# Kernel optimization log

Hardware: AMD Instinct MI355X
Metric: run time of the kernel (lower is better)

## Reference

```python
import jax, jax.numpy as jnp
import numpy as np

H, W, WS, HEADS = 112, 112, 7, 8
DIM, HID = 512, 2048


def _layernorm(x, g, b, eps=1e-5):
    mu = jnp.mean(x, axis=-1, keepdims=True)
    var = jnp.var(x, axis=-1, keepdims=True)
    return (x - mu) * jax.lax.rsqrt(var + eps) * g + b


def _cpe(x, w, b):
    # depthwise 3x3 conv positional encoding with residual; x: [B, L, C]
    B, L, C = x.shape
    img = x.reshape(B, H, W, C)
    feat = jax.lax.conv_general_dilated(
        img, w, window_strides=(1, 1), padding='SAME',
        dimension_numbers=('NHWC', 'HWIO', 'NHWC'), feature_group_count=C) + b
    return x + feat.reshape(B, L, C)


def _window_partition(x):
    # [B, H, W, C] -> [B*nW, ws*ws, C]
    B, _, _, C = x.shape
    x = x.reshape(B, H // WS, WS, W // WS, WS, C)
    x = jnp.transpose(x, (0, 1, 3, 2, 4, 5))
    return x.reshape(-1, WS * WS, C)


def _window_reverse(xw, B):
    # [B*nW, ws*ws, C] -> [B, H*W, C]
    C = xw.shape[-1]
    x = xw.reshape(B, H // WS, W // WS, WS, WS, C)
    x = jnp.transpose(x, (0, 1, 3, 2, 4, 5))
    return x.reshape(B, H * W, C)


def _attention(x, qkv_w, qkv_b, proj_w, proj_b):
    # x: [nW, N, C]; standard MHA within each window
    nW, N, C = x.shape
    d = C // HEADS
    qkv = x @ qkv_w + qkv_b                      # [nW, N, 3C]
    qkv = qkv.reshape(nW, N, 3, HEADS, d)
    q, k, v = qkv[:, :, 0], qkv[:, :, 1], qkv[:, :, 2]  # [nW, N, h, d]
    scale = d ** -0.5
    attn = jnp.einsum('wqhd,wkhd->whqk', q * scale, k)
    attn = jax.nn.softmax(attn, axis=-1)
    out = jnp.einsum('whqk,wkhd->wqhd', attn, v).reshape(nW, N, C)
    return out @ proj_w + proj_b


def setup_inputs() -> dict:
    key = jax.random.key(0)
    ks = jax.random.split(key, 16)
    s = 0.02
    return {
        'x': jax.random.normal(ks[0], (4, H * W, DIM), jnp.float32),
        'cpe0_w': jax.random.normal(ks[1], (3, 3, 1, DIM), jnp.float32) * s,
        'cpe0_b': jnp.zeros((DIM,), jnp.float32),
        'cpe1_w': jax.random.normal(ks[2], (3, 3, 1, DIM), jnp.float32) * s,
        'cpe1_b': jnp.zeros((DIM,), jnp.float32),
        'ln1_g': jnp.ones((DIM,), jnp.float32),
        'ln1_b': jnp.zeros((DIM,), jnp.float32),
        'ln2_g': jnp.ones((DIM,), jnp.float32),
        'ln2_b': jnp.zeros((DIM,), jnp.float32),
        'qkv_w': jax.random.normal(ks[3], (DIM, 3 * DIM), jnp.float32) * s,
        'qkv_b': jnp.zeros((3 * DIM,), jnp.float32),
        'attn_proj_w': jax.random.normal(ks[4], (DIM, DIM), jnp.float32) * s,
        'attn_proj_b': jnp.zeros((DIM,), jnp.float32),
        'fc1_w': jax.random.normal(ks[5], (DIM, HID), jnp.float32) * s,
        'fc1_b': jnp.zeros((HID,), jnp.float32),
        'fc2_w': jax.random.normal(ks[6], (HID, DIM), jnp.float32) * s,
        'fc2_b': jnp.zeros((DIM,), jnp.float32),
    }


def reference(x, cpe0_w, cpe0_b, cpe1_w, cpe1_b, ln1_g, ln1_b, ln2_g, ln2_b,
              qkv_w, qkv_b, attn_proj_w, attn_proj_b, fc1_w, fc1_b, fc2_w, fc2_b):
    B, L, C = x.shape
    shortcut = _cpe(x, cpe0_w, cpe0_b)                 # CPE #1 (with residual)
    h = _layernorm(shortcut, ln1_g, ln1_b)
    h = _window_partition(h.reshape(B, H, W, C))       # [B*nW, 49, C]
    h = _attention(h, qkv_w, qkv_b, attn_proj_w, attn_proj_b)
    h = _window_reverse(h, B)                          # [B, L, C]
    h = shortcut + h
    h = _cpe(h, cpe1_w, cpe1_b)                        # CPE #2 (with residual)
    m = _layernorm(h, ln2_g, ln2_b)
    m = jax.nn.gelu(m @ fc1_w + fc1_b) @ fc2_w + fc2_b
    return h + m
```

## Files before the change

kernel.cpp:

```cpp
#include <hip/hip_runtime.h>
#include <stdint.h>

#define HH 112
#define WW 112
#define CC 512
#define BB 4
#define LLEN (HH*WW)
#define NTOK (BB*LLEN)
#define NHEADS 8
#define HD 64
#define HIDDEN 2048

typedef __bf16 bf16x8 __attribute__((ext_vector_type(8)));
typedef float f32x4 __attribute__((ext_vector_type(4)));
typedef int i32x8 __attribute__((ext_vector_type(8)));
typedef long i64;

__device__ __forceinline__ unsigned short f2bf(float x) {
  uint32_t u = __float_as_uint(x);
  u += 0x7fffu + ((u >> 16) & 1u);
  return (unsigned short)(u >> 16);
}
__device__ __forceinline__ float bf2f(unsigned short h) {
  return __uint_as_float((uint32_t)h << 16);
}
__device__ __forceinline__ int cvt4_fp8(float a, float b, float c, float d) {
  int r = 0;
  r = __builtin_amdgcn_cvt_pk_fp8_f32(a, b, r, false);
  r = __builtin_amdgcn_cvt_pk_fp8_f32(c, d, r, true);
  return r;
}

__device__ __forceinline__ void gload16(const void* gptr, void* lptr) {
  __builtin_amdgcn_global_load_lds(
      (const __attribute__((address_space(1))) void*)gptr,
      (__attribute__((address_space(3))) void*)lptr,
      16, 0, 0);
}

#define WAITV3() asm volatile("s_waitcnt vmcnt(3)" ::: "memory")
#define WAITV4() asm volatile("s_waitcnt vmcnt(4)" ::: "memory")
#define WAITV0() asm volatile("s_waitcnt vmcnt(0)" ::: "memory")
#define BAR() __builtin_amdgcn_s_barrier()
#define WAITL() do { asm volatile("s_waitcnt lgkmcnt(0)" ::: "memory"); \
                     __builtin_amdgcn_sched_barrier(0); } while (0)

__global__ __launch_bounds__(256) void wtranspose8_kernel(
    const float* __restrict__ w, unsigned char* __restrict__ wt, int K, int N) {
  int idx = blockIdx.x * 256 + threadIdx.x;
  if (idx >= K * N) return;
  int n = idx / K, k = idx - n * K;
  float v = w[(size_t)k * N + n] * 32.f;
  int r = __builtin_amdgcn_cvt_pk_fp8_f32(v, v, 0, false);
  wt[idx] = (unsigned char)r;
}

template <int INBF, int OUTBF>
__global__ __launch_bounds__(256) void cpe_ln_kernel(
    const void* __restrict__ xin, const float* __restrict__ w,
    const float* __restrict__ bias, const float* __restrict__ lng,
    const float* __restrict__ lnb, void* __restrict__ outp,
    unsigned char* __restrict__ ln8) {
  const int wid = threadIdx.x >> 6;
  const int lane = threadIdx.x & 63;
  const int xx = blockIdx.x * 4 + wid;
  const int yy = blockIdx.y;
  const int bb = blockIdx.z;
  const int c = lane * 8;

  float acc[8];
  {
    float4 b0 = *(const float4*)(&bias[c]);
    float4 b1 = *(const float4*)(&bias[c + 4]);
    acc[0] = b0.x; acc[1] = b0.y; acc[2] = b0.z; acc[3] = b0.w;
    acc[4] = b1.x; acc[5] = b1.y; acc[6] = b1.z; acc[7] = b1.w;
  }
  float xv[8];

  #pragma unroll
  for (int ky = 0; ky < 3; ky++) {
    int y = yy + ky - 1;
    bool yok = (unsigned)y < (unsigned)HH;
    #pragma unroll
    for (int kx = 0; kx < 3; kx++) {
      int x2 = xx + kx - 1;
      bool ok = yok && ((unsigned)x2 < (unsigned)WW);
      float v[8];
      if (ok) {
        size_t eo = (((size_t)bb * HH + y) * WW + x2) * CC + c;
        if (INBF) {
          uint4 u = *(const uint4*)(&((const unsigned short*)xin)[eo]);
          v[0] = bf2f((unsigned short)(u.x & 0xffff)); v[1] = bf2f((unsigned short)(u.x >> 16));
          v[2] = bf2f((unsigned short)(u.y & 0xffff)); v[3] = bf2f((unsigned short)(u.y >> 16));
          v[4] = bf2f((unsigned short)(u.z & 0xffff)); v[5] = bf2f((unsigned short)(u.z >> 16));
          v[6] = bf2f((unsigned short)(u.w & 0xffff)); v[7] = bf2f((unsigned short)(u.w >> 16));
        } else {
          float4 a = *(const float4*)(&((const float*)xin)[eo]);
          float4 b = *(const float4*)(&((const float*)xin)[eo + 4]);
          v[0] = a.x; v[1] = a.y; v[2] = a.z; v[3] = a.w;
          v[4] = b.x; v[5] = b.y; v[6] = b.z; v[7] = b.w;
        }
      } else {
        #pragma unroll
        for (int e = 0; e < 8; e++) v[e] = 0.f;
      }
      if (ky == 1 && kx == 1) {
        #pragma unroll
        for (int e = 0; e < 8; e++) xv[e] = v[e];
      }
      float4 w0 = *(const float4*)(&w[(ky * 3 + kx) * CC + c]);
      float4 w1 = *(const float4*)(&w[(ky * 3 + kx) * CC + c + 4]);
      acc[0] = fmaf(v[0], w0.x, acc[0]); acc[1] = fmaf(v[1], w0.y, acc[1]);
      acc[2] = fmaf(v[2], w0.z, acc[2]); acc[3] = fmaf(v[3], w0.w, acc[3]);
      acc[4] = fmaf(v[4], w1.x, acc[4]); acc[5] = fmaf(v[5], w1.y, acc[5]);
      acc[6] = fmaf(v[6], w1.z, acc[6]); acc[7] = fmaf(v[7], w1.w, acc[7]);
    }
  }

  float r[8];
  #pragma unroll
  for (int e = 0; e < 8; e++) r[e] = xv[e] + acc[e];

  const size_t o = (((size_t)bb * HH + yy) * WW + xx) * CC + c;
  if (OUTBF) {
    uint4 pk;
    pk.x = (uint32_t)f2bf(r[0]) | ((uint32_t)f2bf(r[1]) << 16);
    pk.y = (uint32_t)f2bf(r[2]) | ((uint32_t)f2bf(r[3]) << 16);
    pk.z = (uint32_t)f2bf(r[4]) | ((uint32_t)f2bf(r[5]) << 16);
    pk.w = (uint32_t)f2bf(r[6]) | ((uint32_t)f2bf(r[7]) << 16);
    *(uint4*)(&((unsigned short*)outp)[o]) = pk;
  } else {
    float4 r0, r1;
    r0.x = r[0]; r0.y = r[1]; r0.z = r[2]; r0.w = r[3];
    r1.x = r[4]; r1.y = r[5]; r1.z = r[6]; r1.w = r[7];
    *(float4*)(&((float*)outp)[o]) = r0;
    *(float4*)(&((float*)outp)[o + 4]) = r1;
  }

  float s = 0.f, ss = 0.f;
  #pragma unroll
  for (int e = 0; e < 8; e++) { s += r[e]; ss += r[e] * r[e]; }
  #pragma unroll
  for (int of = 32; of; of >>= 1) {
    s += __shfl_xor(s, of, 64);
    ss += __shfl_xor(ss, of, 64);
  }
  float mu = s * (1.f / CC);
  float var = ss * (1.f / CC) - mu * mu;
  float rsd = rsqrtf(var + 1e-5f);
  float4 g0 = *(const float4*)(&lng[c]);
  float4 g1 = *(const float4*)(&lng[c + 4]);
  float4 b0 = *(const float4*)(&lnb[c]);
  float4 b1 = *(const float4*)(&lnb[c + 4]);
  float gv[8] = {g0.x, g0.y, g0.z, g0.w, g1.x, g1.y, g1.z, g1.w};
  float bv[8] = {b0.x, b0.y, b0.z, b0.w, b1.x, b1.y, b1.z, b1.w};
  float ov[8];
  #pragma unroll
  for (int e = 0; e < 8; e++) ov[e] = (r[e] - mu) * rsd * gv[e] + bv[e];
  uint2 pk8;
  pk8.x = (uint32_t)cvt4_fp8(ov[0], ov[1], ov[2], ov[3]);
  pk8.y = (uint32_t)cvt4_fp8(ov[4], ov[5], ov[6], ov[7]);
  *(uint2*)(&ln8[o]) = pk8;
}

#define BM 256
#define BN 128
#define BK8 64

template <int MODE, int K>
__global__ __launch_bounds__(512) void gemm8_kernel(
    const unsigned char* __restrict__ A, const unsigned char* __restrict__ BT,
    const float* __restrict__ bias, const unsigned short* __restrict__ resB,
    unsigned short* __restrict__ outB16, int M, int N) {
  __shared__ unsigned char ldsb[49152];
  int nwg = gridDim.x * gridDim.y;
  int flat = blockIdx.y * gridDim.x + blockIdx.x;
  int swz = (flat & 7) * (nwg >> 3) + (flat >> 3);
  int bx = swz % gridDim.x, by = swz / gridDim.x;
  const int bm = by * BM, bn = bx * BN;
  const int t = threadIdx.x;
  const int wid = t >> 6, lane = t & 63;
  const int wr = wid >> 1, wc = wid & 1;
  const int lr = lane & 15, g = lane >> 4;
  const int swr = (lr >> 1) & 3;
  const int rb0 = (((g >> 1)      ) ^ swr) * 16 + (g & 1) * 8;
  const int rb1 = (((g >> 1) + 2) ^ swr) * 16 + (g & 1) * 8;
  const int srow = t >> 2;
  const int scol = (((t & 3) ^ ((t >> 3) & 3)) & 3) * 16;
  const size_t arow0 = (size_t)(bm + srow) * K + scol;
  const size_t arow1 = (size_t)(bm + 128 + srow) * K + scol;
  const size_t brow  = (size_t)(bn + srow) * K + scol;
  const int ldso = wid * 1024;

#define STG8(b, kt) do { \
    gload16(&A[arow0 + (kt)], ldsb + (b) * 16384 + ldso); \
    gload16(&A[arow1 + (kt)], ldsb + (b) * 16384 + 8192 + ldso); \
    gload16(&BT[brow + (kt)], ldsb + 32768 + (b) * 8192 + ldso); } while (0)

  f32x4 acc[4][4] = {};
  constexpr int nt = K / BK8;

  STG8(0, 0);
  STG8(1, BK8);

  #pragma unroll
  for (int tile = 0; tile < nt - 1; ++tile) {
    WAITV3(); BAR();
    const unsigned char* as = ldsb + (tile & 1) * 16384;
    const unsigned char* bs = ldsb + 32768 + (tile & 1) * 8192;
    i64 af0[4], af1[4], bf0[4], bf1[4];
    #pragma unroll
    for (int i = 0; i < 4; i++) {
      const unsigned char* p = &as[(wr * 64 + i * 16 + lr) * BK8];
      af0[i] = *(const i64*)(p + rb0);
      af1[i] = *(const i64*)(p + rb1);
    }
    #pragma unroll
    for (int j = 0; j < 4; j++) {
      const unsigned char* p = &bs[(wc * 64 + j * 16 + lr) * BK8];
      bf0[j] = *(const i64*)(p + rb0);
      bf1[j] = *(const i64*)(p + rb1);
    }
    WAITL();
    BAR();
    if (tile + 2 < nt) STG8(tile & 1, (tile + 2) * BK8);
    __builtin_amdgcn_s_setprio(1);
    #pragma unroll
    for (int i = 0; i < 4; i++)
      #pragma unroll
      for (int j = 0; j < 4; j++) {
        acc[i][j] = __builtin_amdgcn_mfma_f32_16x16x32_fp8_fp8(af0[i], bf0[j], acc[i][j], 0, 0, 0);
        acc[i][j] = __builtin_amdgcn_mfma_f32_16x16x32_fp8_fp8(af1[i], bf1[j], acc[i][j], 0, 0, 0);
      }
    __builtin_amdgcn_s_setprio(0);
  }
  {
    WAITV0(); BAR();
    const unsigned char* as = ldsb + ((nt - 1) & 1) * 16384;
    const unsigned char* bs = ldsb + 32768 + ((nt - 1) & 1) * 8192;
    i64 af0[4], af1[4], bf0[4], bf1[4];
    #pragma unroll
    for (int i = 0; i < 4; i++) {
      const unsigned char* p = &as[(wr * 64 + i * 16 + lr) * BK8];
      af0[i] = *(const i64*)(p + rb0);
      af1[i] = *(const i64*)(p + rb1);
    }
    #pragma unroll
    for (int j = 0; j < 4; j++) {
      const unsigned char* p = &bs[(wc * 64 + j * 16 + lr) * BK8];
      bf0[j] = *(const i64*)(p + rb0);
      bf1[j] = *(const i64*)(p + rb1);
    }
    WAITL();
    #pragma unroll
    for (int i = 0; i < 4; i++)
      #pragma unroll
      for (int j = 0; j < 4; j++) {
        acc[i][j] = __builtin_amdgcn_mfma_f32_16x16x32_fp8_fp8(af0[i], bf0[j], acc[i][j], 0, 0, 0);
        acc[i][j] = __builtin_amdgcn_mfma_f32_16x16x32_fp8_fp8(af1[i], bf1[j], acc[i][j], 0, 0, 0);
      }
  }
#undef STG8

  {
    const float SC = 0.03125f;
    float* eps = (float*)ldsb;
    const int erow = t >> 3;
    const int ecol0 = (t & 7) * 16;
    const int wrow = wr * 16 + (lane >> 4) * 4;
    const int wcol = wc * 64 + lr;
    const int gr_base = bm + (erow >> 4) * 64 + (erow & 15);
    const int gc0 = bn + ecol0;
    float bv[16];
    #pragma unroll
    for (int c4 = 0; c4 < 4; c4++)
      *(float4*)&bv[c4 * 4] = *(const float4*)&bias[gc0 + c4 * 4];
    #pragma unroll
    for (int i = 0; i < 4; i++) {
      __syncthreads();
      #pragma unroll
      for (int j = 0; j < 4; j++)
        #pragma unroll
        for (int r = 0; r < 4; r++)
          eps[(wrow + r) * 132 + wcol + j * 16] = acc[i][j][r];
      __syncthreads();
      float vv[16];
      #pragma unroll
      for (int c4 = 0; c4 < 4; c4++)
        *(float4*)&vv[c4 * 4] = *(const float4*)&eps[erow * 132 + ecol0 + c4 * 4];
      const size_t off = (size_t)(gr_base + i * 16) * N + gc0;
      uint4 r0 = *(const uint4*)&resB[off];
      uint4 r1 = *(const uint4*)&resB[off + 8];
      unsigned short ob[16];
      const uint32_t* rp = (const uint32_t*)&r0;
      #pragma unroll
      for (int c = 0; c < 8; c++) {
        uint32_t u = rp[c >> 1];
        float rv = bf2f((unsigned short)((c & 1) ? (u >> 16) : (u & 0xffff)));
        ob[c] = f2bf(vv[c] * SC + bv[c] + rv);
      }
      const uint32_t* rp1 = (const uint32_t*)&r1;
      #pragma unroll
      for (int c = 0; c < 8; c++) {
        uint32_t u = rp1[c >> 1];
        float rv = bf2f((unsigned short)((c & 1) ? (u >> 16) : (u & 0xffff)));
        ob[8 + c] = f2bf(vv[8 + c] * SC + bv[8 + c] + rv);
      }
      *(uint4*)&outB16[off]     = *(uint4*)&ob[0];
      *(uint4*)&outB16[off + 8] = *(uint4*)&ob[8];
    }
  }
}

__device__ __forceinline__ i32x8 ld_frag128(const unsigned char* base, int row, int g, int lrm7) {
  const uint4 lo = *(const uint4*)(base + row * 128 + (((2 * g)     ^ lrm7) * 16));
  const uint4 hi = *(const uint4*)(base + row * 128 + (((2 * g + 1) ^ lrm7) * 16));
  i32x8 r;
  r[0] = lo.x; r[1] = lo.y; r[2] = lo.z; r[3] = lo.w;
  r[4] = hi.x; r[5] = hi.y; r[6] = hi.z; r[7] = hi.w;
  return r;
}

template <int MODE, int K>
__global__ __launch_bounds__(512) void gemm8mx_kernel(
    const unsigned char* __restrict__ A, const unsigned char* __restrict__ BT,
    const float* __restrict__ bias, const float* __restrict__ res,
    float* __restrict__ outF, unsigned char* __restrict__ outB8,
    int M, int N) {
  __shared__ unsigned char ldsb[65536];
  const int SCALE1 = 0x7F7F7F7F;
  int nwg = gridDim.x * gridDim.y;
  int flat = blockIdx.y * gridDim.x + blockIdx.x;
  int swz = (flat & 7) * (nwg >> 3) + (flat >> 3);
  int bx = swz % gridDim.x, by = swz / gridDim.x;
  const int bm = by * 128, bn = bx * 128;
  const int t = threadIdx.x;
  const int wid = t >> 6, lane = t & 63;
  const int wr = wid >> 2, wc = wid & 3;
  const int lr = lane & 15, g = lane >> 4, lrm7 = lane & 7;
  const int srow8 = lane >> 3;
  const int schunk = ((lane & 7) ^ srow8) * 16;
  const size_t aBase = (size_t)(bm + wid * 16 + srow8) * K + schunk;
  const size_t bBase = (size_t)(bn + wid * 16 + srow8) * K + schunk;
  const size_t row8K = (size_t)8 * K;
  const int ldsl = wid * 2048;

#define STGMX(p, kt) do { \
    gload16(&A[aBase + (kt)],          ldsb + (p) * 16384 + ldsl); \
    gload16(&A[aBase + row8K + (kt)],  ldsb + (p) * 16384 + ldsl + 1024); \
    gload16(&BT[bBase + (kt)],         ldsb + 32768 + (p) * 16384 + ldsl); \
    gload16(&BT[bBase + row8K + (kt)], ldsb + 32768 + (p) * 16384 + ldsl + 1024); } while (0)

  f32x4 acc[4][2] = {};
  constexpr int npt = K / 128;

  STGMX(0, 0);
  STGMX(1, 128);

  #pragma unroll
  for (int pt = 0; pt < npt - 1; ++pt) {
    WAITV4(); BAR();
    const unsigned char* as = ldsb + (pt & 1) * 16384;
    const unsigned char* bs = ldsb + 32768 + (pt & 1) * 16384;
    i32x8 af[4], bf[2];
    #pragma unroll
    for (int i = 0; i < 4; i++)
      af[i] = ld_frag128(as, wr * 64 + i * 16 + lr, g, lrm7);
    #pragma unroll
    for (int j = 0; j < 2; j++)
      bf[j] = ld_frag128(bs, wc * 32 + j * 16 + lr, g, lrm7);
    WAITL();
    BAR();
    if (pt + 2 < npt) STGMX(pt & 1, (pt + 2) * 128);
    __builtin_amdgcn_s_setprio(1);
    #pragma unroll
    for (int i = 0; i < 4; i++)
      #pragma unroll
      for (int j = 0; j < 2; j++)
        acc[i][j] = __builtin_amdgcn_mfma_scale_f32_16x16x128_f8f6f4(
            af[i], bf[j], acc[i][j], 0, 0, 0, SCALE1, 0, SCALE1);
    __builtin_amdgcn_s_setprio(0);
  }
  {
    WAITV0(); BAR();
    const unsigned char* as = ldsb + ((npt - 1) & 1) * 16384;
    const unsigned char* bs = ldsb + 32768 + ((npt - 1) & 1) * 16384;
    i32x8 af[4], bf[2];
    #pragma unroll
    for (int i = 0; i < 4; i++)
      af[i] = ld_frag128(as, wr * 64 + i * 16 + lr, g, lrm7);
    #pragma unroll
    for (int j = 0; j < 2; j++)
      bf[j] = ld_frag128(bs, wc * 32 + j * 16 + lr, g, lrm7);
    WAITL();
    #pragma unroll
    for (int i = 0; i < 4; i++)
      #pragma unroll
      for (int j = 0; j < 2; j++)
        acc[i][j] = __builtin_amdgcn_mfma_scale_f32_16x16x128_f8f6f4(
            af[i], bf[j], acc[i][j], 0, 0, 0, SCALE1, 0, SCALE1);
  }
#undef STGMX

  {
    const float SC = 0.03125f;
    float* eps = (float*)ldsb;
    const int erow = t >> 3;
    const int cb = (t & 7) * 16;
    float4 bv4[4];
    #pragma unroll
    for (int c4 = 0; c4 < 4; c4++)
      bv4[c4] = *(const float4*)&bias[bn + cb + c4 * 4];
    #pragma unroll
    for (int p = 0; p < 2; p++) {
      __syncthreads();
      if (wr == p) {
        #pragma unroll
        for (int i = 0; i < 4; i++)
          #pragma unroll
          for (int j = 0; j < 2; j++)
            #pragma unroll
            for (int r = 0; r < 4; r++)
              eps[(i * 16 + g * 4 + r) * 132 + wc * 32 + j * 16 + lr] = acc[i][j][r];
      }
      __syncthreads();
      const size_t rowoff = (size_t)(bm + p * 64 + erow) * N + bn + cb;
      if (MODE == 1) {
        #pragma unroll
        for (int c4 = 0; c4 < 4; c4++) {
          float4 vv = *(const float4*)&eps[erow * 132 + cb + c4 * 4];
          float4 rv = *(const float4*)&res[rowoff + c4 * 4];
          float4 ov;
          ov.x = vv.x * SC + bv4[c4].x + rv.x;
          ov.y = vv.y * SC + bv4[c4].y + rv.y;
          ov.z = vv.z * SC + bv4[c4].z + rv.z;
          ov.w = vv.w * SC + bv4[c4].w + rv.w;
          *(float4*)&outF[rowoff + c4 * 4] = ov;
        }
      } else {
        uint32_t ob32[4];
        #pragma unroll
        for (int c4 = 0; c4 < 4; c4++) {
          float4 vv = *(const float4*)&eps[erow * 132 + cb + c4 * 4];
          float v0 = vv.x * SC + bv4[c4].x;
          float v1 = vv.y * SC + bv4[c4].y;
          float v2 = vv.z * SC + bv4[c4].z;
          float v3 = vv.w * SC + bv4[c4].w;
          if (MODE == 2) {
            float vin[4] = {v0, v1, v2, v3};
            float gvv[4];
            #pragma unroll
            for (int e = 0; e < 4; e++) {
              float v = vin[e];
              float a2 = v * v;
              float w = v * fmaf(a2, -0.1029436f, -2.3024849f);
              float sg = __builtin_amdgcn_rcpf(1.f + __builtin_amdgcn_exp2f(w));
              gvv[e] = v * sg;
            }
            ob32[c4] = (uint32_t)cvt4_fp8(gvv[0], gvv[1], gvv[2], gvv[3]);
          } else {
            ob32[c4] = (uint32_t)cvt4_fp8(v0, v1, v2, v3);
          }
        }
        *(uint4*)&outB8[rowoff] = *(uint4*)&ob32[0];
      }
    }
  }
}

#define WNS8 72

__global__ __launch_bounds__(64) void attn_mfma8_kernel(
    const unsigned char* __restrict__ qkv, unsigned char* __restrict__ out) {
  __shared__ unsigned char VT[64 * WNS8];
  __shared__ unsigned char Ps[64 * WNS8];
  const int task = blockIdx.x;
  const int win = task >> 3, h = task & 7;
  const int b = win >> 8, wy = (win >> 4) & 15, wx = win & 15;
  const int lane = threadIdx.x;
  const int lr = lane & 15, g = lane >> 4;

  auto tokof = [&](int r) {
    int rr = r > 48 ? 48 : r;
    int y = rr / 7, x2 = rr - y * 7;
    return (size_t)(b * LLEN + (wy * 7 + y) * WW + wx * 7 + x2);
  };

  {
    size_t vbase = tokof(lane) * 1536 + 1024 + h * 64;
    bool valid = lane <= 48;
    #pragma unroll
    for (int c = 0; c < 4; c++) {
      uint4 v = *(const uint4*)(&qkv[vbase + c * 16]);
      const unsigned char* pv = (const unsigned char*)&v;
      #pragma unroll
      for (int e = 0; e < 16; e++)
        VT[(c * 16 + e) * WNS8 + lane] = valid ? pv[e] : (unsigned char)0;
    }
  }

  size_t tok[4];
  #pragma unroll
  for (int i2 = 0; i2 < 4; i2++) tok[i2] = tokof(i2 * 16 + lr);
  i64 Qf[4][2], Kf[4][2];
  #pragma unroll
  for (int i2 = 0; i2 < 4; i2++) {
    size_t base = tok[i2] * 1536 + h * 64 + g * 8;
    #pragma unroll
    for (int ks = 0; ks < 2; ks++) {
      Qf[i2][ks] = *(const i64*)(&qkv[base + ks * 32]);
      Kf[i2][ks] = *(const i64*)(&qkv[base + 512 + ks * 32]);
    }
  }

  f32x4 acc[4][4] = {};
  #pragma unroll
  for (int ks = 0; ks < 2; ks++)
    #pragma unroll
    for (int i2 = 0; i2 < 4; i2++)
      #pragma unroll
      for (int j = 0; j < 4; j++)
        acc[i2][j] = __builtin_amdgcn_mfma_f32_16x16x32_fp8_fp8(Kf[i2][ks], Qf[j][ks], acc[i2][j], 0, 0, 0);

  #pragma unroll
  for (int j = 0; j < 4; j++) {
    float mx = -1e30f;
    #pragma unroll
    for (int i2 = 0; i2 < 4; i2++)
      #pragma unroll
      for (int r = 0; r < 4; r++) {
        int k = 16 * i2 + 4 * g + r;
        mx = fmaxf(mx, (k <= 48) ? acc[i2][j][r] : -1e30f);
      }
    mx = fmaxf(mx, __shfl_xor(mx, 16, 64));
    mx = fmaxf(mx, __shfl_xor(mx, 32, 64));
    float p[4][4];
    float sum = 0.f;
    #pragma unroll
    for (int i2 = 0; i2 < 4; i2++)
      #pragma unroll
      for (int r = 0; r < 4; r++) {
        int k = 16 * i2 + 4 * g + r;
        float e = (k <= 48) ? __expf(0.125f * (acc[i2][j][r] - mx)) : 0.f;
        p[i2][r] = e; sum += e;
      }
    sum += __shfl_xor(sum, 16, 64);
    sum += __shfl_xor(sum, 32, 64);
    float inv = 1.f / sum;
    int q = 16 * j + lr;
    #pragma unroll
    for (int i2 = 0; i2 < 4; i2++) {
      uint32_t w = (uint32_t)cvt4_fp8(p[i2][0] * inv, p[i2][1] * inv,
                                      p[i2][2] * inv, p[i2][3] * inv);
      *(uint32_t*)(&Ps[q * WNS8 + 16 * i2 + 4 * g]) = w;
    }
  }

  __syncthreads();

  f32x4 o[4][4] = {};
  #pragma unroll
  for (int ks = 0; ks < 2; ks++) {
    i64 Pf[4], Vf[4];
    #pragma unroll
    for (int i2 = 0; i2 < 4; i2++)
      Pf[i2] = *(const i64*)(&Ps[(16 * i2 + lr) * WNS8 + ks * 32 + g * 8]);
    #pragma unroll
    for (int j = 0; j < 4; j++)
      Vf[j] = *(const i64*)(&VT[(16 * j + lr) * WNS8 + ks * 32 + g * 8]);
    #pragma unroll
    for (int i2 = 0; i2 < 4; i2++)
      #pragma unroll
      for (int j = 0; j < 4; j++)
        o[i2][j] = __builtin_amdgcn_mfma_f32_16x16x32_fp8_fp8(Pf[i2], Vf[j], o[i2][j], 0, 0, 0);
  }

  #pragma unroll
  for (int i2 = 0; i2 < 4; i2++)
    #pragma unroll
    for (int r = 0; r < 4; r++) {
      int q = 16 * i2 + 4 * g + r;
      if (q <= 48) {
        size_t obase = tokof(q) * 512 + h * 64 + lr;
        #pragma unroll
        for (int j = 0; j < 4; j++) {
          float v = o[i2][j][r];
          int rr = __builtin_amdgcn_cvt_pk_fp8_f32(v, v, 0, false);
          out[obase + 16 * j] = (unsigned char)rr;
        }
      }
    }
}

extern "C" void kernel_launch(void* const* d_in, const int* in_sizes, int n_in,
                              void* d_out, int out_size, void* d_ws, size_t ws_size,
                              hipStream_t stream) {
  const float* x      = (const float*)d_in[0];
  const float* cpe0_w = (const float*)d_in[1];
  const float* cpe0_b = (const float*)d_in[2];
  const float* cpe1_w = (const float*)d_in[3];
  const float* cpe1_b = (const float*)d_in[4];
  const float* ln1_g  = (const float*)d_in[5];
  const float* ln1_b  = (const float*)d_in[6];
  const float* ln2_g  = (const float*)d_in[7];
  const float* ln2_b  = (const float*)d_in[8];
  const float* qkv_w  = (const float*)d_in[9];
  const float* qkv_b  = (const float*)d_in[10];
  const float* proj_w = (const float*)d_in[11];
  const float* proj_b = (const float*)d_in[12];
  const float* fc1_w  = (const float*)d_in[13];
  const float* fc1_b  = (const float*)d_in[14];
  const float* fc2_w  = (const float*)d_in[15];
  const float* fc2_b  = (const float*)d_in[16];
  float* out = (float*)d_out;
  char* ws = (char*)d_ws;

  unsigned char*  qkvwT8 = (unsigned char*)(ws + 0);
  unsigned char*  projwT8 = (unsigned char*)(ws + 1048576);
  unsigned char*  fc1wT8 = (unsigned char*)(ws + 2097152);
  unsigned char*  fc2wT8 = (unsigned char*)(ws + 4194304);
  unsigned short* shortcB = (unsigned short*)(ws + 6291456);
  unsigned char*  lnb8   = (unsigned char*)(ws + 109051904);
  unsigned char*  qkvb8  = (unsigned char*)(ws + 160432128);
  unsigned char*  attnb8 = (unsigned char*)(ws + 314572800);
  unsigned char*  gelub8 = (unsigned char*)(ws + 160432128);
  float* h2 = out;

  wtranspose8_kernel<<<(512 * 1536 + 255) / 256, 256, 0, stream>>>(qkv_w, qkvwT8, 512, 1536);
  wtranspose8_kernel<<<(512 * 512 + 255) / 256, 256, 0, stream>>>(proj_w, projwT8, 512, 512);
  wtranspose8_kernel<<<(512 * 2048 + 255) / 256, 256, 0, stream>>>(fc1_w, fc1wT8, 512, 2048);
  wtranspose8_kernel<<<(2048 * 512 + 255) / 256, 256, 0, stream>>>(fc2_w, fc2wT8, 2048, 512);

  cpe_ln_kernel<0, 1><<<dim3(28, 112, BB), 256, 0, stream>>>(x, cpe0_w, cpe0_b,
      ln1_g, ln1_b, shortcB, lnb8);
  gemm8mx_kernel<0, 512><<<dim3(12, 392), 512, 0, stream>>>(lnb8, qkvwT8, qkv_b, nullptr,
      nullptr, qkvb8, NTOK, 1536);
  attn_mfma8_kernel<<<8192, 64, 0, stream>>>(qkvb8, attnb8);
  gemm8_kernel<3, 512><<<dim3(4, 196), 512, 0, stream>>>(attnb8, projwT8, proj_b,
      shortcB, shortcB, NTOK, 512);
  cpe_ln_kernel<1, 0><<<dim3(28, 112, BB), 256, 0, stream>>>(shortcB, cpe1_w, cpe1_b,
      ln2_g, ln2_b, h2, lnb8);
  gemm8mx_kernel<2, 512><<<dim3(16, 392), 512, 0, stream>>>(lnb8, fc1wT8, fc1_b, nullptr,
      nullptr, gelub8, NTOK, 2048);
  gemm8mx_kernel<1, 2048><<<dim3(4, 392), 512, 0, stream>>>(gelub8, fc2wT8, fc2_b, h2,
      out, nullptr, NTOK, 512);
}
```

Measured before the change: 533.0 us.

## Store second CPE output as bf16 residual and merge weight-transpose launches

The second CPE+LN kernel now writes its residual in bf16 to a workspace buffer instead of fp32 into the output. The final fc2 GEMM (new MODE 4) reads that bf16 residual and unpacks it in the epilogue. This halves the residual's write and read traffic, at the cost of bf16 rounding on the residual path. The four weight-transpose launches are also fused into one kernel to cut launch overhead.

```diff
diff --git a/kernel.cpp b/kernel.cpp
--- a/kernel.cpp
+++ b/kernel.cpp
@@ -45,21 +45,28 @@
 #define WAITL() do { asm volatile("s_waitcnt lgkmcnt(0)" ::: "memory"); \
                      __builtin_amdgcn_sched_barrier(0); } while (0)
 
-__global__ __launch_bounds__(256) void wtranspose8_kernel(
-    const float* __restrict__ w, unsigned char* __restrict__ wt, int K, int N) {
+__global__ __launch_bounds__(256) void wtall_kernel(
+    const float* __restrict__ qkv_w, const float* __restrict__ proj_w,
+    const float* __restrict__ fc1_w, const float* __restrict__ fc2_w,
+    unsigned char* __restrict__ o0, unsigned char* __restrict__ o1,
+    unsigned char* __restrict__ o2, unsigned char* __restrict__ o3) {
   int idx = blockIdx.x * 256 + threadIdx.x;
-  if (idx >= K * N) return;
+  const float* w; unsigned char* o; int K, N;
+  if (idx < 786432)        { w = qkv_w;  o = o0; K = 512;  N = 1536; }
+  else if (idx < 1048576)  { w = proj_w; o = o1; K = 512;  N = 512;  idx -= 786432; }
+  else if (idx < 2097152)  { w = fc1_w;  o = o2; K = 512;  N = 2048; idx -= 1048576; }
+  else                     { w = fc2_w;  o = o3; K = 2048; N = 512;  idx -= 2097152; }
   int n = idx / K, k = idx - n * K;
   float v = w[(size_t)k * N + n] * 32.f;
   int r = __builtin_amdgcn_cvt_pk_fp8_f32(v, v, 0, false);
-  wt[idx] = (unsigned char)r;
-}
-
-template <int INBF, int OUTBF>
+  o[idx] = (unsigned char)r;
+}
+
+template <int INBF>
 __global__ __launch_bounds__(256) void cpe_ln_kernel(
     const void* __restrict__ xin, const float* __restrict__ w,
     const float* __restrict__ bias, const float* __restrict__ lng,
-    const float* __restrict__ lnb, void* __restrict__ outp,
+    const float* __restrict__ lnb, unsigned short* __restrict__ outB,
     unsigned char* __restrict__ ln8) {
   const int wid = threadIdx.x >> 6;
   const int lane = threadIdx.x & 63;
@@ -122,19 +129,13 @@
   for (int e = 0; e < 8; e++) r[e] = xv[e] + acc[e];
 
   const size_t o = (((size_t)bb * HH + yy) * WW + xx) * CC + c;
-  if (OUTBF) {
+  {
     uint4 pk;
     pk.x = (uint32_t)f2bf(r[0]) | ((uint32_t)f2bf(r[1]) << 16);
     pk.y = (uint32_t)f2bf(r[2]) | ((uint32_t)f2bf(r[3]) << 16);
     pk.z = (uint32_t)f2bf(r[4]) | ((uint32_t)f2bf(r[5]) << 16);
     pk.w = (uint32_t)f2bf(r[6]) | ((uint32_t)f2bf(r[7]) << 16);
-    *(uint4*)(&((unsigned short*)outp)[o]) = pk;
-  } else {
-    float4 r0, r1;
-    r0.x = r[0]; r0.y = r[1]; r0.z = r[2]; r0.w = r[3];
-    r1.x = r[4]; r1.y = r[5]; r1.z = r[6]; r1.w = r[7];
-    *(float4*)(&((float*)outp)[o]) = r0;
-    *(float4*)(&((float*)outp)[o + 4]) = r1;
+    *(uint4*)(&outB[o]) = pk;
   }
 
   float s = 0.f, ss = 0.f;
@@ -324,7 +325,7 @@
 template <int MODE, int K>
 __global__ __launch_bounds__(512) void gemm8mx_kernel(
     const unsigned char* __restrict__ A, const unsigned char* __restrict__ BT,
-    const float* __restrict__ bias, const float* __restrict__ res,
+    const float* __restrict__ bias, const unsigned short* __restrict__ resB,
     float* __restrict__ outF, unsigned char* __restrict__ outB8,
     int M, int N) {
   __shared__ unsigned char ldsb[65536];
@@ -425,16 +426,30 @@
       }
       __syncthreads();
       const size_t rowoff = (size_t)(bm + p * 64 + erow) * N + bn + cb;
-      if (MODE == 1) {
+      if (MODE == 4) {
+        uint4 r0 = *(const uint4*)&resB[rowoff];
+        uint4 r1 = *(const uint4*)&resB[rowoff + 8];
+        float rvv[16];
+        const uint32_t* rp0 = (const uint32_t*)&r0;
+        const uint32_t* rp1 = (const uint32_t*)&r1;
+        #pragma unroll
+        for (int c = 0; c < 8; c++) {
+          uint32_t u = rp0[c >> 1];
+          rvv[c] = bf2f((unsigned short)((c & 1) ? (u >> 16) : (u & 0xffff)));
+        }
+        #pragma unroll
+        for (int c = 0; c < 8; c++) {
+          uint32_t u = rp1[c >> 1];
+          rvv[8 + c] = bf2f((unsigned short)((c & 1) ? (u >> 16) : (u & 0xffff)));
+        }
         #pragma unroll
         for (int c4 = 0; c4 < 4; c4++) {
           float4 vv = *(const float4*)&eps[erow * 132 + cb + c4 * 4];
-          float4 rv = *(const float4*)&res[rowoff + c4 * 4];
           float4 ov;
-          ov.x = vv.x * SC + bv4[c4].x + rv.x;
-          ov.y = vv.y * SC + bv4[c4].y + rv.y;
-          ov.z = vv.z * SC + bv4[c4].z + rv.z;
-          ov.w = vv.w * SC + bv4[c4].w + rv.w;
+          ov.x = vv.x * SC + bv4[c4].x + rvv[c4 * 4 + 0];
+          ov.y = vv.y * SC + bv4[c4].y + rvv[c4 * 4 + 1];
+          ov.z = vv.z * SC + bv4[c4].z + rvv[c4 * 4 + 2];
+          ov.w = vv.w * SC + bv4[c4].w + rvv[c4 * 4 + 3];
           *(float4*)&outF[rowoff + c4 * 4] = ov;
         }
       } else {
@@ -615,33 +630,31 @@
   float* out = (float*)d_out;
   char* ws = (char*)d_ws;
 
-  unsigned char*  qkvwT8 = (unsigned char*)(ws + 0);
+  unsigned char*  qkvwT8  = (unsigned char*)(ws + 0);
   unsigned char*  projwT8 = (unsigned char*)(ws + 1048576);
-  unsigned char*  fc1wT8 = (unsigned char*)(ws + 2097152);
-  unsigned char*  fc2wT8 = (unsigned char*)(ws + 4194304);
+  unsigned char*  fc1wT8  = (unsigned char*)(ws + 2097152);
+  unsigned char*  fc2wT8  = (unsigned char*)(ws + 4194304);
   unsigned short* shortcB = (unsigned short*)(ws + 6291456);
-  unsigned char*  lnb8   = (unsigned char*)(ws + 109051904);
-  unsigned char*  qkvb8  = (unsigned char*)(ws + 160432128);
-  unsigned char*  attnb8 = (unsigned char*)(ws + 314572800);
-  unsigned char*  gelub8 = (unsigned char*)(ws + 160432128);
-  float* h2 = out;
-
-  wtranspose8_kernel<<<(512 * 1536 + 255) / 256, 256, 0, stream>>>(qkv_w, qkvwT8, 512, 1536);
-  wtranspose8_kernel<<<(512 * 512 + 255) / 256, 256, 0, stream>>>(proj_w, projwT8, 512, 512);
-  wtranspose8_kernel<<<(512 * 2048 + 255) / 256, 256, 0, stream>>>(fc1_w, fc1wT8, 512, 2048);
-  wtranspose8_kernel<<<(2048 * 512 + 255) / 256, 256, 0, stream>>>(fc2_w, fc2wT8, 2048, 512);
-
-  cpe_ln_kernel<0, 1><<<dim3(28, 112, BB), 256, 0, stream>>>(x, cpe0_w, cpe0_b,
+  unsigned char*  lnb8    = (unsigned char*)(ws + 109051904);
+  unsigned char*  qkvb8   = (unsigned char*)(ws + 160432128);
+  unsigned char*  attnb8  = (unsigned char*)(ws + 314572800);
+  unsigned char*  gelub8  = (unsigned char*)(ws + 160432128);
+  unsigned short* h2B     = (unsigned short*)(ws + 314572800);
+
+  wtall_kernel<<<12288, 256, 0, stream>>>(qkv_w, proj_w, fc1_w, fc2_w,
+                                          qkvwT8, projwT8, fc1wT8, fc2wT8);
+
+  cpe_ln_kernel<0><<<dim3(28, 112, BB), 256, 0, stream>>>(x, cpe0_w, cpe0_b,
       ln1_g, ln1_b, shortcB, lnb8);
-  gemm8mx_kernel<0, 512><<<dim3(12, 392), 512, 0, stream>>>(lnb8, qkvwT8, qkv_b, nullptr,
-      nullptr, qkvb8, NTOK, 1536);
+  gemm8mx_kernel<0, 512><<<dim3(12, 392), 512, 0, stream>>>(lnb8, qkvwT8, qkv_b,
+      nullptr, nullptr, qkvb8, NTOK, 1536);
   attn_mfma8_kernel<<<8192, 64, 0, stream>>>(qkvb8, attnb8);
   gemm8_kernel<3, 512><<<dim3(4, 196), 512, 0, stream>>>(attnb8, projwT8, proj_b,
       shortcB, shortcB, NTOK, 512);
-  cpe_ln_kernel<1, 0><<<dim3(28, 112, BB), 256, 0, stream>>>(shortcB, cpe1_w, cpe1_b,
-      ln2_g, ln2_b, h2, lnb8);
-  gemm8mx_kernel<2, 512><<<dim3(16, 392), 512, 0, stream>>>(lnb8, fc1wT8, fc1_b, nullptr,
-      nullptr, gelub8, NTOK, 2048);
-  gemm8mx_kernel<1, 2048><<<dim3(4, 392), 512, 0, stream>>>(gelub8, fc2wT8, fc2_b, h2,
-      out, nullptr, NTOK, 512);
-}
+  cpe_ln_kernel<1><<<dim3(28, 112, BB), 256, 0, stream>>>(shortcB, cpe1_w, cpe1_b,
+      ln2_g, ln2_b, h2B, lnb8);
+  gemm8mx_kernel<2, 512><<<dim3(16, 392), 512, 0, stream>>>(lnb8, fc1wT8, fc1_b,
+      nullptr, nullptr, gelub8, NTOK, 2048);
+  gemm8mx_kernel<4, 2048><<<dim3(4, 392), 512, 0, stream>>>(gelub8, fc2wT8, fc2_b,
+      h2B, out, nullptr, NTOK, 512);
+}
```

New measurement: 517.1 us, median of 3. -3.0%, faster.
